# Optimization experiments

Measured on AMD Instinct MI355X. Metric: run time of the kernel, lower is better.

Reference implementation:

```python
import jax, jax.numpy as jnp
import numpy as np

B, IN_CH, OUT_CH, H, W = 8, 64, 128, 128, 128
K = 3          # i2h kernel
L = 5          # number of flow fields
FLOW_HID = 32  # hidden channels of flow generator
NEG_SLOPE = 0.2


def _conv(x, w, b, pad):
    y = jax.lax.conv_general_dilated(x, w, (1, 1), [(pad, pad), (pad, pad)],
                                     dimension_numbers=('NCHW', 'OIHW', 'NCHW'))
    return y + b[None, :, None, None]


def _leaky(x):
    return jnp.where(x >= 0, x, NEG_SLOPE * x)


def _bilinear(img, px, py):
    # img [B,C,H,W]; px,py [B,H,W] pixel coords. Bilinear, zero padding,
    # align_corners=True semantics (normalization by W-1 cancels out -> pixel coords).
    Bs, C, Hs, Ws = img.shape
    x0 = jnp.floor(px); y0 = jnp.floor(py)
    wx = px - x0; wy = py - y0
    bidx = jnp.arange(Bs)[:, None, None]
    def g(xi, yi):
        valid = (xi >= 0) & (xi <= Ws - 1) & (yi >= 0) & (yi <= Hs - 1)
        xc = jnp.clip(xi, 0, Ws - 1).astype(jnp.int32)
        yc = jnp.clip(yi, 0, Hs - 1).astype(jnp.int32)
        v = img[bidx, :, yc, xc]  # [B,H,W,C]
        return jnp.where(valid[..., None], v, jnp.zeros((), img.dtype))
    out = ((1 - wy)[..., None] * ((1 - wx)[..., None] * g(x0, y0) + wx[..., None] * g(x0 + 1, y0))
           + wy[..., None] * ((1 - wx)[..., None] * g(x0, y0 + 1) + wx[..., None] * g(x0 + 1, y0 + 1)))
    return out.transpose(0, 3, 1, 2)  # [B,C,H,W]


def _trajgru_step(x, h, i2h_w, i2h_b, i2f_w, i2f_b, h2f_w, h2f_b, flow_w, flow_b, ret_w, ret_b):
    Bs, F, Hs, Ws = h.shape
    # flow generator
    f1 = _leaky(_conv(x, i2f_w, i2f_b, 2) + _conv(h, h2f_w, h2f_b, 2))
    flows = _conv(f1, flow_w, flow_b, 2).reshape(Bs, L, 2, Hs, Ws)
    # warp hidden state: wrap(h, -flow) => sample at grid - flow
    xx = jnp.arange(Ws, dtype=x.dtype)[None, :]
    yy = jnp.arange(Hs, dtype=x.dtype)[:, None]
    px = xx[None, None] - flows[:, :, 0]  # [B,L,H,W]
    py = yy[None, None] - flows[:, :, 1]
    warped = jax.vmap(_bilinear, in_axes=(None, 1, 1), out_axes=1)(h, px, py)  # [B,L,F,H,W]
    h2h = _conv(warped.reshape(Bs, L * F, Hs, Ws), ret_w, ret_b, 0)  # [B,3F,H,W]
    i2h = _conv(x, i2h_w, i2h_b, K // 2)                             # [B,3F,H,W]
    r = jax.nn.sigmoid(i2h[:, :F] + h2h[:, :F])
    u = jax.nn.sigmoid(i2h[:, F:2 * F] + h2h[:, F:2 * F])
    new_mem = _leaky(i2h[:, 2 * F:] + r * h2h[:, 2 * F:])
    return u * h + (1 - u) * new_mem


def setup_inputs() -> dict:
    key = jax.random.key(0)
    ks = jax.random.split(key, 16)
    d = {}
    d['x'] = jax.random.normal(ks[0], (B, IN_CH, H, W), jnp.float32)
    d['h_prev1'] = jnp.zeros((B, OUT_CH, H, W), jnp.float32)
    d['h_prev2'] = jnp.zeros((B, OUT_CH, H, W), jnp.float32)
    def mk(k, shape):
        return jax.random.normal(k, shape, jnp.float32) * 0.05
    i = 1
    for s, cin in (('1', IN_CH), ('2', OUT_CH)):
        d['i2h_w' + s] = mk(ks[i], (3 * OUT_CH, cin, K, K)); i += 1
        d['i2h_b' + s] = jnp.zeros((3 * OUT_CH,), jnp.float32)
        d['i2f_w' + s] = mk(ks[i], (FLOW_HID, cin, 5, 5)); i += 1
        d['i2f_b' + s] = jnp.zeros((FLOW_HID,), jnp.float32)
        d['h2f_w' + s] = mk(ks[i], (FLOW_HID, OUT_CH, 5, 5)); i += 1
        d['h2f_b' + s] = jnp.zeros((FLOW_HID,), jnp.float32)
        d['flow_w' + s] = mk(ks[i], (2 * L, FLOW_HID, 5, 5)); i += 1
        d['flow_b' + s] = jnp.zeros((2 * L,), jnp.float32)
        d['ret_w' + s] = mk(ks[i], (3 * OUT_CH, L * OUT_CH, 1, 1)); i += 1
        d['ret_b' + s] = jnp.zeros((3 * OUT_CH,), jnp.float32)
    return d


def reference(x, h_prev1, h_prev2,
              i2h_w1, i2h_b1, i2f_w1, i2f_b1, h2f_w1, h2f_b1, flow_w1, flow_b1, ret_w1, ret_b1,
              i2h_w2, i2h_b2, i2f_w2, i2f_b2, h2f_w2, h2f_b2, flow_w2, flow_b2, ret_w2, ret_b2):
    h1 = _trajgru_step(x, h_prev1, i2h_w1, i2h_b1, i2f_w1, i2f_b1, h2f_w1, h2f_b1,
                       flow_w1, flow_b1, ret_w1, ret_b1)
    h2 = _trajgru_step(h1, h_prev2, i2h_w2, i2h_b2, i2f_w2, i2f_b2, h2f_w2, h2f_b2,
                       flow_w2, flow_b2, ret_w2, ret_b2)
    return h2
```

## Files before the change

kernel.cpp:

```cpp
#include <hip/hip_runtime.h>
#include <hip/hip_bf16.h>
#include <cstdint>
#include <cstddef>

#define HH 128
#define WW 128
#define HW 16384
#define NEGS 0.2f

typedef __attribute__((ext_vector_type(8))) short short8;
typedef __attribute__((ext_vector_type(4))) short s16x4;
typedef __attribute__((ext_vector_type(4))) float f32x4;

__device__ __forceinline__ float leakyf(float v) { return v >= 0.f ? v : NEGS * v; }
__device__ __forceinline__ float sigmf_(float v) { return 1.f / (1.f + __expf(-v)); }
__device__ __forceinline__ float bf2f(short s) {
  union { float f; unsigned u; } x;
  x.u = ((unsigned)(unsigned short)s) << 16;
  return x.f;
}
__device__ __forceinline__ short f2bf(float v) {
  __hip_bfloat16 h = __float2bfloat16(v);
  return *(short*)&h;
}

__global__ __launch_bounds__(256) void k_pack(const float* __restrict__ src,
                                              __hip_bfloat16* __restrict__ dst,
                                              int OC, int CINs, int T, int kbase,
                                              int KK) {
  int i = blockIdx.x * 256 + threadIdx.x;
  if (i >= OC * CINs * T) return;
  int t = i % T;
  int c = (i / T) % CINs;
  int oc = i / (T * CINs);
  dst[(size_t)oc * KK + kbase + t * CINs + c] = __float2bfloat16(src[i]);
}

template <int CH>
__global__ __launch_bounds__(256) void k_cast_nhwc(const float* __restrict__ in,
                                                   __hip_bfloat16* __restrict__ out) {
  __shared__ float t[32][33];
  int bx = blockIdx.x;
  int cx = blockIdx.y;
  int bz = blockIdx.z;
  int b = bz >> 7, y = bz & 127;
  int tx = threadIdx.x & 31, tg = threadIdx.x >> 5;
#pragma unroll
  for (int i = 0; i < 4; ++i) {
    int c = cx * 32 + tg * 4 + i;
    t[tg * 4 + i][tx] = in[(((size_t)b * CH + c) * 128 + y) * 128 + bx * 32 + tx];
  }
  __syncthreads();
#pragma unroll
  for (int i = 0; i < 4; ++i) {
    int x = bx * 32 + tg * 4 + i;
    size_t pix = ((size_t)b * 128 + y) * 128 + x;
    out[pix * CH + cx * 32 + tx] = __float2bfloat16(t[tx][tg * 4 + i]);
  }
}

__global__ __launch_bounds__(256) void k_tonchw(const float* __restrict__ in,
                                                float* __restrict__ out) {
  __shared__ float t[32][33];
  int bx = blockIdx.x;
  int cx = blockIdx.y;
  int bz = blockIdx.z;
  int b = bz >> 7, y = bz & 127;
  int tx = threadIdx.x & 31, tg = threadIdx.x >> 5;
#pragma unroll
  for (int i = 0; i < 4; ++i) {
    int x = bx * 32 + tg * 4 + i;
    t[tg * 4 + i][tx] = in[(((size_t)b * 128 + y) * 128 + x) * 128 + cx * 32 + tx];
  }
  __syncthreads();
#pragma unroll
  for (int i = 0; i < 4; ++i) {
    int c = cx * 32 + tg * 4 + i;
    out[(((size_t)b * 128 + c) * 128 + y) * 128 + bx * 32 + tx] = t[tx][tg * 4 + i];
  }
}

template <int CS, int NFR, int KK>
__device__ __forceinline__ void mc_seg(const short* __restrict__ src,
                                       const short* __restrict__ wrow,
                                       int kbase, int dy, int dx,
                                       const int* py_r, const int* px_m,
                                       int lk, f32x4 (&acc)[4][NFR]) {
  const short* aptr[4];
  bool av[4];
#pragma unroll
  for (int fm = 0; fm < 4; ++fm) {
    int yy = (py_r[fm] & 127) + dy;
    int bb = py_r[fm] >> 7;
    int xx = px_m[fm] + dx;
    bool ok = ((unsigned)yy < 128u) && ((unsigned)xx < 128u);
    av[fm] = ok;
    int ycl = ok ? yy : 0;
    int xcl = ok ? xx : 0;
    size_t pix = ((size_t)(bb << 7) + ycl) * 128 + xcl;
    aptr[fm] = src + pix * CS + lk;
  }
  const short8 z = {0, 0, 0, 0, 0, 0, 0, 0};
#pragma unroll
  for (int c0 = 0; c0 < CS; c0 += 32) {
    short8 bf[NFR];
#pragma unroll
    for (int fn = 0; fn < NFR; ++fn)
      bf[fn] = *(const short8*)&wrow[(size_t)fn * 16 * KK + kbase + c0];
    short8 af[4];
#pragma unroll
    for (int fm = 0; fm < 4; ++fm) {
      short8 v = *(const short8*)(aptr[fm] + c0);
      af[fm] = av[fm] ? v : z;
    }
#pragma unroll
    for (int fm = 0; fm < 4; ++fm)
#pragma unroll
      for (int fn = 0; fn < NFR; ++fn)
        acc[fm][fn] = __builtin_amdgcn_mfma_f32_16x16x32_bf16(
            af[fm], bf[fn], acc[fm][fn], 0, 0, 0);
  }
}

template <int CIN1, int CIN2, int RAD, int BN, bool LEAKY, int MODE>
__global__ __launch_bounds__(256) void k_mconv(
    const short* __restrict__ in1, const short* __restrict__ in2,
    const short* __restrict__ wb, const float* __restrict__ bias1,
    const float* __restrict__ bias2, void* __restrict__ outp,
    void* __restrict__ outp2, int nout, int ostride) {
  constexpr int KD = 2 * RAD + 1;
  constexpr int T = KD * KD;
  constexpr int KK = T * (CIN1 + CIN2);
  constexpr int WN = (BN >= 32) ? 2 : 1;
  constexpr int ROWS = (WN == 2) ? 1 : 2;
  constexpr int NFR = BN / (16 * WN);

  int tid = threadIdx.x, lane = tid & 63, wid = tid >> 6;
  int wm = wid / WN, wn = wid % WN;
  int l15 = lane & 15, lk = (lane >> 4) * 8;
  int r0 = blockIdx.x * ROWS;
  int ocb = blockIdx.y * BN + wn * (NFR * 16);

  f32x4 acc[4][NFR];
#pragma unroll
  for (int i = 0; i < 4; ++i)
#pragma unroll
    for (int j = 0; j < NFR; ++j) {
      acc[i][j][0] = 0.f; acc[i][j][1] = 0.f;
      acc[i][j][2] = 0.f; acc[i][j][3] = 0.f;
    }

  int py_r[4], px_m[4];
#pragma unroll
  for (int fm = 0; fm < 4; ++fm) {
    int m = wm * 64 + fm * 16 + l15;
    py_r[fm] = r0 + (m >> 7);
    px_m[fm] = m & 127;
  }

  const short* wrow = wb + (size_t)(ocb + l15) * KK + lk;

#pragma unroll 1
  for (int s = 0; s < T; ++s) {
    int dy = s / KD - RAD, dx = s % KD - RAD;
    mc_seg<CIN1, NFR, KK>(in1, wrow, s * CIN1, dy, dx, py_r, px_m, lk, acc);
  }
  if constexpr (CIN2 > 0) {
#pragma unroll 1
    for (int s = 0; s < T; ++s) {
      int dy = s / KD - RAD, dx = s % KD - RAD;
      mc_seg<CIN2, NFR, KK>(in2, wrow, T * CIN1 + s * CIN2, dy, dx, py_r, px_m,
                            lk, acc);
    }
  }

#pragma unroll
  for (int fn = 0; fn < NFR; ++fn) {
    int ocx = ocb + fn * 16 + l15;
    float bv = 0.f;
    if (ocx < nout) {
      bv = bias1[ocx];
      if (bias2) bv += bias2[ocx];
    }
#pragma unroll
    for (int fm = 0; fm < 4; ++fm) {
#pragma unroll
      for (int j = 0; j < 4; ++j) {
        int m = wm * 64 + fm * 16 + (lane >> 4) * 4 + j;
        int row = r0 + (m >> 7);
        size_t pix = (size_t)row * 128 + (m & 127);
        float v = acc[fm][fn][j] + bv;
        if (LEAKY) v = leakyf(v);
        if (ocx < nout) {
          if constexpr (MODE == 1)
            ((__hip_bfloat16*)outp)[pix * ostride + ocx] = __float2bfloat16(v);
          else if constexpr (MODE == 0)
            ((float*)outp)[pix * ostride + ocx] = v;
          else {
            if (ocx < 256)
              ((float*)outp)[pix * 384 + ocx] += v;
            else
              ((float*)outp2)[pix * 128 + (ocx - 256)] = v;
          }
        }
      }
    }
  }
}

__global__ __launch_bounds__(256) void k_warp5(
    const __hip_bfloat16* __restrict__ h_t, const float* __restrict__ flows,
    __hip_bfloat16* __restrict__ wout) {
  int t = threadIdx.x;
  int c = t & 127;
  size_t n = (size_t)blockIdx.x * 2 + (t >> 7);
  int b = (int)(n >> 14);
  int p = (int)(n & 16383);
  int y = p >> 7, x = p & 127;
  const __hip_bfloat16* base = h_t + (size_t)b * HW * 128;
#pragma unroll 1
  for (int l = 0; l < 5; ++l) {
    float fx = flows[n * 16 + 2 * l];
    float fy = flows[n * 16 + 2 * l + 1];
    float px = (float)x - fx;
    float py = (float)y - fy;
    float x0f = floorf(px), y0f = floorf(py);
    float wx = px - x0f, wy = py - y0f;
    int x0 = (int)x0f, y0i = (int)y0f;
    float v00 = 0.f, v10 = 0.f, v01 = 0.f, v11 = 0.f;
    if ((unsigned)x0 <= 127u && (unsigned)y0i <= 127u)
      v00 = __bfloat162float(base[((size_t)y0i * WW + x0) * 128 + c]);
    if ((unsigned)(x0 + 1) <= 127u && (unsigned)y0i <= 127u)
      v10 = __bfloat162float(base[((size_t)y0i * WW + (x0 + 1)) * 128 + c]);
    if ((unsigned)x0 <= 127u && (unsigned)(y0i + 1) <= 127u)
      v01 = __bfloat162float(base[((size_t)(y0i + 1) * WW + x0) * 128 + c]);
    if ((unsigned)(x0 + 1) <= 127u && (unsigned)(y0i + 1) <= 127u)
      v11 = __bfloat162float(base[((size_t)(y0i + 1) * WW + (x0 + 1)) * 128 + c]);
    float v = (1.f - wy) * ((1.f - wx) * v00 + wx * v10) +
              wy * ((1.f - wx) * v01 + wx * v11);
    wout[n * 640 + l * 128 + c] = __float2bfloat16(v);
  }
}

template <bool FINAL>
__global__ __launch_bounds__(256) void k_gates2(
    const float* __restrict__ i2h, const float* __restrict__ h2h,
    const __hip_bfloat16* __restrict__ hpt, void* __restrict__ outp) {
  int tid = threadIdx.x;
  size_t n = (size_t)blockIdx.x * 8 + (tid >> 5);
  int c4 = (tid & 31) * 4;
  const float* irow = i2h + n * 384;
  f32x4 a0 = *(const f32x4*)(irow + c4);
  f32x4 a1 = *(const f32x4*)(irow + 128 + c4);
  f32x4 a2 = *(const f32x4*)(irow + 256 + c4);
  f32x4 b2 = *(const f32x4*)(h2h + n * 128 + c4);
  s16x4 hv = *(const s16x4*)((const short*)hpt + n * 128 + c4);
  if (FINAL) {
    f32x4 o;
#pragma unroll
    for (int j = 0; j < 4; ++j) {
      float r = sigmf_(a0[j]), u = sigmf_(a1[j]);
      float nm = leakyf(fmaf(r, b2[j], a2[j]));
      o[j] = u * bf2f(hv[j]) + (1.f - u) * nm;
    }
    *(f32x4*)((float*)outp + n * 128 + c4) = o;
  } else {
    s16x4 o;
#pragma unroll
    for (int j = 0; j < 4; ++j) {
      float r = sigmf_(a0[j]), u = sigmf_(a1[j]);
      float nm = leakyf(fmaf(r, b2[j], a2[j]));
      o[j] = f2bf(u * bf2f(hv[j]) + (1.f - u) * nm);
    }
    *(s16x4*)((short*)outp + n * 128 + c4) = o;
  }
}

extern "C" void kernel_launch(void* const* d_in, const int* in_sizes, int n_in,
                              void* d_out, int out_size, void* d_ws, size_t ws_size,
                              hipStream_t stream) {
  const float* x       = (const float*)d_in[0];
  const float* hp1     = (const float*)d_in[1];
  const float* hp2     = (const float*)d_in[2];
  const float* i2h_w1  = (const float*)d_in[3];
  const float* i2h_b1  = (const float*)d_in[4];
  const float* i2f_w1  = (const float*)d_in[5];
  const float* i2f_b1  = (const float*)d_in[6];
  const float* h2f_w1  = (const float*)d_in[7];
  const float* h2f_b1  = (const float*)d_in[8];
  const float* flow_w1 = (const float*)d_in[9];
  const float* flow_b1 = (const float*)d_in[10];
  const float* ret_w1  = (const float*)d_in[11];
  const float* ret_b1  = (const float*)d_in[12];
  const float* i2h_w2  = (const float*)d_in[13];
  const float* i2h_b2  = (const float*)d_in[14];
  const float* i2f_w2  = (const float*)d_in[15];
  const float* i2f_b2  = (const float*)d_in[16];
  const float* h2f_w2  = (const float*)d_in[17];
  const float* h2f_b2  = (const float*)d_in[18];
  const float* flow_w2 = (const float*)d_in[19];
  const float* flow_b2 = (const float*)d_in[20];
  const float* ret_w2  = (const float*)d_in[21];
  const float* ret_b2  = (const float*)d_in[22];
  float* out = (float*)d_out;

  const size_t nWb3_1 = (size_t)384 * 576;
  const size_t nWb3_2 = (size_t)384 * 1152;
  const size_t nWbf1  = (size_t)32 * 4800;
  const size_t nWbf2  = (size_t)32 * 6400;
  const size_t nWfl   = (size_t)16 * 800;
  const size_t nWret  = (size_t)384 * 640;
  const size_t wtot = nWb3_1 + nWb3_2 + nWbf1 + nWbf2 + 2 * nWfl + 2 * nWret;

  int NBC = 8;
  while (NBC > 1 && wtot * 2 + (size_t)3968 * NBC * HW > ws_size)
    NBC >>= 1;
  const int npixc = NBC * HW;

  __hip_bfloat16* wbase = (__hip_bfloat16*)d_ws;
  __hip_bfloat16* Wb3_1 = wbase;
  __hip_bfloat16* Wb3_2 = Wb3_1 + nWb3_1;
  __hip_bfloat16* Wbf1  = Wb3_2 + nWb3_2;
  __hip_bfloat16* Wbf2  = Wbf1 + nWbf1;
  __hip_bfloat16* Wfl1  = Wbf2 + nWbf2;
  __hip_bfloat16* Wfl2  = Wfl1 + nWfl;
  __hip_bfloat16* Wret1 = Wfl2 + nWfl;
  __hip_bfloat16* Wret2 = Wret1 + nWret;

  char* abase = (char*)(Wret2 + nWret);
  float* i2hbuf = (float*)abase;
  float* h2hbuf = i2hbuf + (size_t)npixc * 384;
  __hip_bfloat16* warpb5 = (__hip_bfloat16*)(h2hbuf + (size_t)npixc * 128);
  __hip_bfloat16* h_t = warpb5 + (size_t)npixc * 640;
  __hip_bfloat16* xb  = h_t + (size_t)npixc * 128;
  __hip_bfloat16* f1b = xb + (size_t)npixc * 128;
  float* flowsb = (float*)(f1b + (size_t)npixc * 32);
  float* go = (float*)warpb5;

  dim3 blk(256);
  auto packs = [&](const float* src, __hip_bfloat16* dst, int OC, int CINs,
                   int T, int kbase, int KK) {
    int n = OC * CINs * T;
    k_pack<<<dim3((n + 255) / 256), blk, 0, stream>>>(src, dst, OC, CINs, T,
                                                      kbase, KK);
  };
  packs(i2h_w1, Wb3_1, 384, 64, 9, 0, 576);
  packs(i2h_w2, Wb3_2, 384, 128, 9, 0, 1152);
  packs(i2f_w1, Wbf1, 32, 64, 25, 0, 4800);
  packs(h2f_w1, Wbf1, 32, 128, 25, 1600, 4800);
  packs(i2f_w2, Wbf2, 32, 128, 25, 0, 6400);
  packs(h2f_w2, Wbf2, 32, 128, 25, 3200, 6400);
  packs(flow_w1, Wfl1, 10, 32, 25, 0, 800);
  packs(flow_w2, Wfl2, 10, 32, 25, 0, 800);
  packs(ret_w1, Wret1, 384, 640, 1, 0, 640);
  packs(ret_w2, Wret2, 384, 640, 1, 0, 640);

  for (int b0 = 0; b0 < 8; b0 += NBC) {
    const float* xc   = x + (size_t)b0 * 64 * HW;
    const float* hp1c = hp1 + (size_t)b0 * 128 * HW;
    const float* hp2c = hp2 + (size_t)b0 * 128 * HW;

    k_cast_nhwc<128><<<dim3(4, 4, NBC * 128), blk, 0, stream>>>(hp1c, h_t);
    k_cast_nhwc<64><<<dim3(4, 2, NBC * 128), blk, 0, stream>>>(xc, xb);
    k_mconv<64, 128, 2, 32, true, 1><<<dim3(NBC * 128, 1), blk, 0, stream>>>(
        (const short*)xb, (const short*)h_t, (const short*)Wbf1, i2f_b1,
        h2f_b1, f1b, nullptr, 32, 32);
    k_mconv<32, 0, 2, 16, false, 0><<<dim3(NBC * 64, 1), blk, 0, stream>>>(
        (const short*)f1b, nullptr, (const short*)Wfl1, flow_b1, nullptr,
        flowsb, nullptr, 10, 16);
    k_mconv<64, 0, 1, 128, false, 0><<<dim3(NBC * 128, 3), blk, 0, stream>>>(
        (const short*)xb, nullptr, (const short*)Wb3_1, i2h_b1, nullptr,
        i2hbuf, nullptr, 384, 384);
    k_warp5<<<dim3(npixc / 2), blk, 0, stream>>>(h_t, flowsb, warpb5);
    k_mconv<640, 0, 0, 128, false, 2><<<dim3(NBC * 128, 3), blk, 0, stream>>>(
        (const short*)warpb5, nullptr, (const short*)Wret1, ret_b1, nullptr,
        i2hbuf, h2hbuf, 384, 384);
    k_gates2<false><<<dim3(npixc / 8), blk, 0, stream>>>(i2hbuf, h2hbuf, h_t, xb);

    k_cast_nhwc<128><<<dim3(4, 4, NBC * 128), blk, 0, stream>>>(hp2c, h_t);
    k_mconv<128, 128, 2, 32, true, 1><<<dim3(NBC * 128, 1), blk, 0, stream>>>(
        (const short*)xb, (const short*)h_t, (const short*)Wbf2, i2f_b2,
        h2f_b2, f1b, nullptr, 32, 32);
    k_mconv<32, 0, 2, 16, false, 0><<<dim3(NBC * 64, 1), blk, 0, stream>>>(
        (const short*)f1b, nullptr, (const short*)Wfl2, flow_b2, nullptr,
        flowsb, nullptr, 10, 16);
    k_mconv<128, 0, 1, 128, false, 0><<<dim3(NBC * 128, 3), blk, 0, stream>>>(
        (const short*)xb, nullptr, (const short*)Wb3_2, i2h_b2, nullptr,
        i2hbuf, nullptr, 384, 384);
    k_warp5<<<dim3(npixc / 2), blk, 0, stream>>>(h_t, flowsb, warpb5);
    k_mconv<640, 0, 0, 128, false, 2><<<dim3(NBC * 128, 3), blk, 0, stream>>>(
        (const short*)warpb5, nullptr, (const short*)Wret2, ret_b2, nullptr,
        i2hbuf, h2hbuf, 384, 384);
    k_gates2<true><<<dim3(npixc / 8), blk, 0, stream>>>(i2hbuf, h2hbuf, h_t, go);
    k_tonchw<<<dim3(4, 4, NBC * 128), blk, 0, stream>>>(go, out + (size_t)b0 * 128 * HW);
  }
}
```

Measured before the change: 2.981 ms.

## Split-K flow-generator 5x5 convs across waves with atomic accumulation and finalize pass

Replaces the narrow-output 5x5 flow-generator convolutions (32 and 10 output channels) with a split-K kernel. Each wave handles a strided subset of (tap, channel-chunk) pairs for 64 pixels and atomically adds its partial sums into a zeroed fp32 buffer. A separate finalize kernel then adds biases and applies leaky ReLU and the bf16 or fp32 conversion. This targets low parallelism and occupancy in the small-N convs, where few blocks each ran long serial K loops. The cost is memsets, atomic traffic, an extra pass and more workspace.

```diff
diff --git a/kernel.cpp b/kernel.cpp
--- a/kernel.cpp
+++ b/kernel.cpp
@@ -81,6 +81,129 @@
 }
 
 template <int CS, int NFR, int KK>
+__device__ __forceinline__ void fc_do(const short* __restrict__ src,
+                                      const short* __restrict__ wrow,
+                                      int wk, int c0, int tap,
+                                      int b, int y, int xb0, int l15, int lk,
+                                      f32x4 (&acc)[4][NFR]) {
+  int dy = tap / 5 - 2, dx = tap % 5 - 2;
+  int yy = y + dy;
+  bool yok = (unsigned)yy < 128u;
+  short8 bf[NFR];
+#pragma unroll
+  for (int fn = 0; fn < NFR; ++fn)
+    bf[fn] = *(const short8*)&wrow[(size_t)(fn * 16) * KK + wk];
+  const short8 z = {0, 0, 0, 0, 0, 0, 0, 0};
+  const short* rbase = src + ((size_t)b * 16384 + (size_t)(yok ? yy : 0) * 128) * CS + c0 + lk;
+  short8 af[4];
+#pragma unroll
+  for (int fm = 0; fm < 4; ++fm) {
+    int xx = xb0 + fm * 16 + l15 + dx;
+    bool ok = yok && ((unsigned)xx < 128u);
+    short8 v = *(const short8*)(rbase + (size_t)(ok ? xx : 0) * CS);
+    af[fm] = ok ? v : z;
+  }
+#pragma unroll
+  for (int fm = 0; fm < 4; ++fm)
+#pragma unroll
+    for (int fn = 0; fn < NFR; ++fn)
+      acc[fm][fn] = __builtin_amdgcn_mfma_f32_16x16x32_bf16(
+          af[fm], bf[fn], acc[fm][fn], 0, 0, 0);
+}
+
+template <int CIN1, int CIN2, int NFR, int NSY>
+__global__ __launch_bounds__(256) void k_fconv(
+    const short* __restrict__ in1, const short* __restrict__ in2,
+    const short* __restrict__ wb, float* __restrict__ acco) {
+  constexpr int KK = 25 * (CIN1 + CIN2);
+  constexpr int C1 = CIN1 / 32;
+  constexpr int C2 = (CIN2 > 0) ? CIN2 / 32 : 1;
+  constexpr int NS = 4 * NSY;
+  int tid = threadIdx.x, lane = tid & 63, w = tid >> 6;
+  int l15 = lane & 15, lk = (lane >> 4) * 8;
+  int subset = blockIdx.y * 4 + w;
+  int p0 = blockIdx.x * 64;
+  int b = p0 >> 14;
+  int y = (p0 >> 7) & 127;
+  int xb0 = p0 & 127;
+
+  f32x4 acc[4][NFR];
+#pragma unroll
+  for (int i = 0; i < 4; ++i)
+#pragma unroll
+    for (int j = 0; j < NFR; ++j) {
+      acc[i][j][0] = 0.f; acc[i][j][1] = 0.f;
+      acc[i][j][2] = 0.f; acc[i][j][3] = 0.f;
+    }
+
+  const short* wrow = wb + (size_t)l15 * KK + lk;
+
+  for (int ci = subset; ci < 25 * C1; ci += NS) {
+    int tap = ci / C1;
+    int c0 = (ci % C1) * 32;
+    fc_do<CIN1, NFR, KK>(in1, wrow, tap * CIN1 + c0, c0, tap, b, y, xb0, l15,
+                         lk, acc);
+  }
+  if constexpr (CIN2 > 0) {
+    for (int ci = subset; ci < 25 * C2; ci += NS) {
+      int tap = ci / C2;
+      int c0 = (ci % C2) * 32;
+      fc_do<CIN2, NFR, KK>(in2, wrow, 25 * CIN1 + tap * CIN2 + c0, c0, tap, b,
+                           y, xb0, l15, lk, acc);
+    }
+  }
+
+#pragma unroll
+  for (int fn = 0; fn < NFR; ++fn) {
+    int ocx = fn * 16 + l15;
+#pragma unroll
+    for (int fm = 0; fm < 4; ++fm)
+#pragma unroll
+      for (int j = 0; j < 4; ++j) {
+        int m = fm * 16 + (lane >> 4) * 4 + j;
+        atomicAdd(&acco[(size_t)(p0 + m) * (NFR * 16) + ocx], acc[fm][fn][j]);
+      }
+  }
+}
+
+template <int CW, bool LEAKY, bool OUTBF16>
+__global__ __launch_bounds__(256) void k_ffin(const float* __restrict__ acc,
+                                              const float* __restrict__ b1,
+                                              const float* __restrict__ b2,
+                                              void* __restrict__ outp,
+                                              int nvalid) {
+  size_t gid = (size_t)blockIdx.x * 256 + threadIdx.x;
+  int c4 = (int)((gid * 4) & (CW - 1));
+  f32x4 v = *(const f32x4*)(acc + gid * 4);
+  if (OUTBF16) {
+    s16x4 o;
+#pragma unroll
+    for (int j = 0; j < 4; ++j) {
+      int c = c4 + j;
+      float bv = b1[c] + (b2 ? b2[c] : 0.f);
+      float r = v[j] + bv;
+      if (LEAKY) r = leakyf(r);
+      o[j] = f2bf(r);
+    }
+    *(s16x4*)((short*)outp + gid * 4) = o;
+  } else {
+    f32x4 o;
+#pragma unroll
+    for (int j = 0; j < 4; ++j) {
+      int c = c4 + j;
+      float r = 0.f;
+      if (c < nvalid) {
+        float bv = b1[c] + (b2 ? b2[c] : 0.f);
+        r = v[j] + bv;
+        if (LEAKY) r = leakyf(r);
+      }
+      o[j] = r;
+    }
+    *(f32x4*)((float*)outp + gid * 4) = o;
+  }
+}
+
+template <int CS, int NFR, int KK>
 __device__ __forceinline__ void mc_seg(const short* __restrict__ src,
                                        const short* __restrict__ wrow,
                                        int kbase, int dy, int dx,
@@ -122,23 +245,21 @@
   }
 }
 
-template <int CIN1, int CIN2, int RAD, int BN, bool LEAKY, int MODE>
+template <int CIN1, int RAD, int BN, int MODE>
 __global__ __launch_bounds__(256) void k_mconv(
-    const short* __restrict__ in1, const short* __restrict__ in2,
-    const short* __restrict__ wb, const float* __restrict__ bias1,
-    const float* __restrict__ bias2, void* __restrict__ outp,
+    const short* __restrict__ in1, const short* __restrict__ wb,
+    const float* __restrict__ bias1, void* __restrict__ outp,
     void* __restrict__ outp2, int nout, int ostride) {
   constexpr int KD = 2 * RAD + 1;
   constexpr int T = KD * KD;
-  constexpr int KK = T * (CIN1 + CIN2);
-  constexpr int WN = (BN >= 32) ? 2 : 1;
-  constexpr int ROWS = (WN == 2) ? 1 : 2;
-  constexpr int NFR = BN / (16 * WN);
+  constexpr int KK = T * CIN1;
+  constexpr int WN = 2;
+  constexpr int NFR = BN / 32;
 
   int tid = threadIdx.x, lane = tid & 63, wid = tid >> 6;
   int wm = wid / WN, wn = wid % WN;
   int l15 = lane & 15, lk = (lane >> 4) * 8;
-  int r0 = blockIdx.x * ROWS;
+  int r0 = blockIdx.x;
   int ocb = blockIdx.y * BN + wn * (NFR * 16);
 
   f32x4 acc[4][NFR];
@@ -165,23 +286,11 @@
     int dy = s / KD - RAD, dx = s % KD - RAD;
     mc_seg<CIN1, NFR, KK>(in1, wrow, s * CIN1, dy, dx, py_r, px_m, lk, acc);
   }
-  if constexpr (CIN2 > 0) {
-#pragma unroll 1
-    for (int s = 0; s < T; ++s) {
-      int dy = s / KD - RAD, dx = s % KD - RAD;
-      mc_seg<CIN2, NFR, KK>(in2, wrow, T * CIN1 + s * CIN2, dy, dx, py_r, px_m,
-                            lk, acc);
-    }
-  }
 
 #pragma unroll
   for (int fn = 0; fn < NFR; ++fn) {
     int ocx = ocb + fn * 16 + l15;
-    float bv = 0.f;
-    if (ocx < nout) {
-      bv = bias1[ocx];
-      if (bias2) bv += bias2[ocx];
-    }
+    float bv = bias1[ocx];
 #pragma unroll
     for (int fm = 0; fm < 4; ++fm) {
 #pragma unroll
@@ -190,18 +299,13 @@
         int row = r0 + (m >> 7);
         size_t pix = (size_t)row * 128 + (m & 127);
         float v = acc[fm][fn][j] + bv;
-        if (LEAKY) v = leakyf(v);
-        if (ocx < nout) {
-          if constexpr (MODE == 1)
-            ((__hip_bfloat16*)outp)[pix * ostride + ocx] = __float2bfloat16(v);
-          else if constexpr (MODE == 0)
-            ((float*)outp)[pix * ostride + ocx] = v;
-          else {
-            if (ocx < 256)
-              ((float*)outp)[pix * 384 + ocx] += v;
-            else
-              ((float*)outp2)[pix * 128 + (ocx - 256)] = v;
-          }
+        if constexpr (MODE == 0)
+          ((float*)outp)[pix * ostride + ocx] = v;
+        else {
+          if (ocx < 256)
+            ((float*)outp)[pix * 384 + ocx] += v;
+          else
+            ((float*)outp2)[pix * 128 + (ocx - 256)] = v;
         }
       }
     }
@@ -313,7 +417,7 @@
   const size_t wtot = nWb3_1 + nWb3_2 + nWbf1 + nWbf2 + 2 * nWfl + 2 * nWret;
 
   int NBC = 8;
-  while (NBC > 1 && wtot * 2 + (size_t)3968 * NBC * HW > ws_size)
+  while (NBC > 1 && wtot * 2 + (size_t)4096 * NBC * HW > ws_size)
     NBC >>= 1;
   const int npixc = NBC * HW;
 
@@ -335,6 +439,7 @@
   __hip_bfloat16* xb  = h_t + (size_t)npixc * 128;
   __hip_bfloat16* f1b = xb + (size_t)npixc * 128;
   float* flowsb = (float*)(f1b + (size_t)npixc * 32);
+  float* facc = flowsb + (size_t)npixc * 16;
   float* go = (float*)warpb5;
 
   dim3 blk(256);
@@ -362,35 +467,39 @@
 
     k_cast_nhwc<128><<<dim3(4, 4, NBC * 128), blk, 0, stream>>>(hp1c, h_t);
     k_cast_nhwc<64><<<dim3(4, 2, NBC * 128), blk, 0, stream>>>(xc, xb);
-    k_mconv<64, 128, 2, 32, true, 1><<<dim3(NBC * 128, 1), blk, 0, stream>>>(
-        (const short*)xb, (const short*)h_t, (const short*)Wbf1, i2f_b1,
-        h2f_b1, f1b, nullptr, 32, 32);
-    k_mconv<32, 0, 2, 16, false, 0><<<dim3(NBC * 64, 1), blk, 0, stream>>>(
-        (const short*)f1b, nullptr, (const short*)Wfl1, flow_b1, nullptr,
-        flowsb, nullptr, 10, 16);
-    k_mconv<64, 0, 1, 128, false, 0><<<dim3(NBC * 128, 3), blk, 0, stream>>>(
-        (const short*)xb, nullptr, (const short*)Wb3_1, i2h_b1, nullptr,
-        i2hbuf, nullptr, 384, 384);
+    hipMemsetAsync(facc, 0, (size_t)npixc * 32 * 4, stream);
+    k_fconv<64, 128, 2, 2><<<dim3(npixc / 64, 2), blk, 0, stream>>>(
+        (const short*)xb, (const short*)h_t, (const short*)Wbf1, facc);
+    k_ffin<32, true, true><<<dim3(npixc * 32 / 1024), blk, 0, stream>>>(
+        facc, i2f_b1, h2f_b1, f1b, 32);
+    hipMemsetAsync(facc, 0, (size_t)npixc * 16 * 4, stream);
+    k_fconv<32, 0, 1, 1><<<dim3(npixc / 64, 1), blk, 0, stream>>>(
+        (const short*)f1b, nullptr, (const short*)Wfl1, facc);
+    k_ffin<16, false, false><<<dim3(npixc * 16 / 1024), blk, 0, stream>>>(
+        facc, flow_b1, nullptr, flowsb, 10);
+    k_mconv<64, 1, 128, 0><<<dim3(NBC * 128, 3), blk, 0, stream>>>(
+        (const short*)xb, (const short*)Wb3_1, i2h_b1, i2hbuf, nullptr, 384, 384);
     k_warp5<<<dim3(npixc / 2), blk, 0, stream>>>(h_t, flowsb, warpb5);
-    k_mconv<640, 0, 0, 128, false, 2><<<dim3(NBC * 128, 3), blk, 0, stream>>>(
-        (const short*)warpb5, nullptr, (const short*)Wret1, ret_b1, nullptr,
-        i2hbuf, h2hbuf, 384, 384);
+    k_mconv<640, 0, 128, 2><<<dim3(NBC * 128, 3), blk, 0, stream>>>(
+        (const short*)warpb5, (const short*)Wret1, ret_b1, i2hbuf, h2hbuf, 384, 384);
     k_gates2<false><<<dim3(npixc / 8), blk, 0, stream>>>(i2hbuf, h2hbuf, h_t, xb);
 
     k_cast_nhwc<128><<<dim3(4, 4, NBC * 128), blk, 0, stream>>>(hp2c, h_t);
-    k_mconv<128, 128, 2, 32, true, 1><<<dim3(NBC * 128, 1), blk, 0, stream>>>(
-        (const short*)xb, (const short*)h_t, (const short*)Wbf2, i2f_b2,
-        h2f_b2, f1b, nullptr, 32, 32);
-    k_mconv<32, 0, 2, 16, false, 0><<<dim3(NBC * 64, 1), blk, 0, stream>>>(
-        (const short*)f1b, nullptr, (const short*)Wfl2, flow_b2, nullptr,
-        flowsb, nullptr, 10, 16);
-    k_mconv<128, 0, 1, 128, false, 0><<<dim3(NBC * 128, 3), blk, 0, stream>>>(
-        (const short*)xb, nullptr, (const short*)Wb3_2, i2h_b2, nullptr,
-        i2hbuf, nullptr, 384, 384);
+    hipMemsetAsync(facc, 0, (size_t)npixc * 32 * 4, stream);
+    k_fconv<128, 128, 2, 2><<<dim3(npixc / 64, 2), blk, 0, stream>>>(
+        (const short*)xb, (const short*)h_t, (const short*)Wbf2, facc);
+    k_ffin<32, true, true><<<dim3(npixc * 32 / 1024), blk, 0, stream>>>(
+        facc, i2f_b2, h2f_b2, f1b, 32);
+    hipMemsetAsync(facc, 0, (size_t)npixc * 16 * 4, stream);
+    k_fconv<32, 0, 1, 1><<<dim3(npixc / 64, 1), blk, 0, stream>>>(
+        (const short*)f1b, nullptr, (const short*)Wfl2, facc);
+    k_ffin<16, false, false><<<dim3(npixc * 16 / 1024), blk, 0, stream>>>(
+        facc, flow_b2, nullptr, flowsb, 10);
+    k_mconv<128, 1, 128, 0><<<dim3(NBC * 128, 3), blk, 0, stream>>>(
+        (const short*)xb, (const short*)Wb3_2, i2h_b2, i2hbuf, nullptr, 384, 384);
     k_warp5<<<dim3(npixc / 2), blk, 0, stream>>>(h_t, flowsb, warpb5);
-    k_mconv<640, 0, 0, 128, false, 2><<<dim3(NBC * 128, 3), blk, 0, stream>>>(
-        (const short*)warpb5, nullptr, (const short*)Wret2, ret_b2, nullptr,
-        i2hbuf, h2hbuf, 384, 384);
+    k_mconv<640, 0, 128, 2><<<dim3(NBC * 128, 3), blk, 0, stream>>>(
+        (const short*)warpb5, (const short*)Wret2, ret_b2, i2hbuf, h2hbuf, 384, 384);
     k_gates2<true><<<dim3(npixc / 8), blk, 0, stream>>>(i2hbuf, h2hbuf, h_t, go);
     k_tonchw<<<dim3(4, 4, NBC * 128), blk, 0, stream>>>(go, out + (size_t)b0 * 128 * HW);
   }
```

Result: no change. 3.039 ms (+1.9%).
